# Performance work log

Hardware: AMD Instinct MI355X
Metric: run time of the kernel (lower is better)

Reference implementation:

```python
import jax, jax.numpy as jnp
import numpy as np

MODEL_SIZE = 1024
N_HEAD = 16
D_K = MODEL_SIZE // N_HEAD
B, S = 2, 2048


def setup_inputs() -> dict:
    key = jax.random.key(0)
    ks = jax.random.split(key, 10)
    scale = 1.0 / np.sqrt(MODEL_SIZE)
    q = jax.random.normal(ks[0], (B, S, MODEL_SIZE), dtype=jnp.float32)
    k = jax.random.normal(ks[1], (B, S, MODEL_SIZE), dtype=jnp.float32)
    v = jax.random.normal(ks[2], (B, S, MODEL_SIZE), dtype=jnp.float32)
    mask = jax.random.bernoulli(ks[3], 0.1, (B, S, S))
    Wq = jax.random.normal(ks[4], (MODEL_SIZE, MODEL_SIZE), dtype=jnp.float32) * scale
    bq = jnp.zeros((MODEL_SIZE,), dtype=jnp.float32)
    Wout = jax.random.normal(ks[5], (MODEL_SIZE, MODEL_SIZE), dtype=jnp.float32) * scale
    bout = jnp.zeros((MODEL_SIZE,), dtype=jnp.float32)
    gamma = jnp.ones((MODEL_SIZE,), dtype=jnp.float32)
    beta = jnp.zeros((MODEL_SIZE,), dtype=jnp.float32)
    return {"q": q, "k": k, "v": v, "mask": mask, "Wq": Wq, "bq": bq,
            "Wout": Wout, "bout": bout, "gamma": gamma, "beta": beta}


def _split_heads(x, seq_len):
    # [B, S, D] -> [B, S, h, d_k] -> [B, h, S, d_k] -> [B*h, S, d_k]
    b = x.shape[0]
    return x.reshape(b, seq_len, N_HEAD, D_K).transpose(0, 2, 1, 3).reshape(b * N_HEAD, seq_len, D_K)


def reference(q, k, v, mask, Wq, bq, Wout, bout, gamma, beta):
    residual = q
    len_q, len_k = q.shape[1], k.shape[1]
    # NOTE: faithful to source — linear_q projects q, k AND v.
    qp = _split_heads(q @ Wq.T + bq, len_q)
    kp = _split_heads(k @ Wq.T + bq, len_k)
    vp = _split_heads(v @ Wq.T + bq, len_k)
    # scores: [B*h, len_q, len_k], scale = sqrt(model_size) per source quirk
    attn = jnp.einsum('bqd,bkd->bqk', qp, kp) / jnp.sqrt(jnp.float32(MODEL_SIZE))
    # mask.repeat(h,1,1): tiles head-major -> [h*B, len_q, len_k]
    mask_t = jnp.tile(mask, (N_HEAD, 1, 1))
    attn = jnp.where(mask_t, jnp.float32(-1e18), attn)
    w = jax.nn.softmax(attn, axis=-1)
    out = jnp.einsum('bqk,bkd->bqd', w, vp)  # [B*h, len_q, d_k]
    b = residual.shape[0]
    out = out.reshape(b, N_HEAD, len_q, D_K).transpose(0, 2, 1, 3).reshape(b, len_q, MODEL_SIZE)
    out = out @ Wout.T + bout
    x = residual + out
    mu = jnp.mean(x, axis=-1, keepdims=True)
    var = jnp.var(x, axis=-1, keepdims=True)
    out = (x - mu) / jnp.sqrt(var + 1e-6) * gamma + beta
    return (out, w)
```

## Files before the change

### kernel.cpp

```cpp
#include <hip/hip_runtime.h>
#include <hip/hip_bf16.h>

#define SEQ 2048
#define DIM 1024
#define NH 16
#define DK 64
#define NBH 32
#define MROWS 4096
#define BM 128
#define BN 128
#define BK 32

typedef __attribute__((ext_vector_type(8))) short bf16x8_t;
typedef __attribute__((ext_vector_type(4))) float f32x4_t;

__device__ __forceinline__ unsigned short f2bf(float f) {
  union { float f; unsigned u; } v; v.f = f;
  unsigned r = v.u + 0x7FFFu + ((v.u >> 16) & 1u);
  return (unsigned short)(r >> 16);
}

__device__ __forceinline__ void gload16(const unsigned short* g, unsigned short* l) {
  __builtin_amdgcn_global_load_lds((const __attribute__((address_space(1))) void*)g,
                                   (__attribute__((address_space(3))) void*)l, 16, 0, 0);
}

struct Cvt5 {
  const float* src[5];
  unsigned short* dst[5];
  int n4[5];
};

__global__ __launch_bounds__(256) void cvt5_kernel(Cvt5 P) {
  int i = blockIdx.x * 256 + threadIdx.x;
  int off = 0;
#pragma unroll
  for (int s = 0; s < 5; ++s) {
    int n4 = P.n4[s];
    int j = i - off;
    if (j >= 0 && j < n4) {
      float4 v = reinterpret_cast<const float4*>(P.src[s])[j];
      ushort4 o = make_ushort4(f2bf(v.x), f2bf(v.y), f2bf(v.z), f2bf(v.w));
      reinterpret_cast<ushort4*>(P.dst[s])[j] = o;
    }
    off += n4;
  }
}

__global__ void detect_mask_kernel(const unsigned int* m, int* flag) {
  unsigned acc = 0;
  for (int i = threadIdx.x; i < 2048; i += 64)
    acc |= (m[i] & 0xFFFFFF00u);
  unsigned long long b = __ballot(acc != 0);
  if (threadIdx.x == 0) *flag = (b != 0ull) ? 1 : 0;
}

__global__ __launch_bounds__(256) void cvt_mask_kernel(const void* msrc, unsigned char* mdst, const int* flag) {
  int i = blockIdx.x * 256 + threadIdx.x;
  if (*flag) {
    reinterpret_cast<uchar4*>(mdst)[i] = reinterpret_cast<const uchar4*>(msrc)[i];
  } else {
    int4 v = reinterpret_cast<const int4*>(msrc)[i];
    reinterpret_cast<uchar4*>(mdst)[i] =
        make_uchar4((unsigned char)(v.x != 0), (unsigned char)(v.y != 0),
                    (unsigned char)(v.z != 0), (unsigned char)(v.w != 0));
  }
}

__device__ __forceinline__ void gemm_core_128(const unsigned short* A, const unsigned short* Wb,
                                              unsigned short* AL, unsigned short* BL,
                                              f32x4_t acc[4][4], int wv, int lane,
                                              int wr, int wc, int lr, int lg) {
  for (int k0 = 0; k0 < DIM; k0 += BK) {
    if (k0) __syncthreads();
#pragma unroll
    for (int j = 0; j < 2; ++j) {
      const int e = wv * 1024 + j * 512 + lane * 8;
      const int row = e >> 5, kk = e & 31;
      gload16(A + (size_t)row * DIM + k0 + kk, AL + wv * 1024 + j * 512);
      gload16(Wb + (size_t)row * DIM + k0 + kk, BL + wv * 1024 + j * 512);
    }
    __syncthreads();
    bf16x8_t a[4], b[4];
#pragma unroll
    for (int m = 0; m < 4; ++m)
      a[m] = *reinterpret_cast<const bf16x8_t*>(AL + (wr * 64 + m * 16 + lr) * BK + lg * 8);
#pragma unroll
    for (int n = 0; n < 4; ++n)
      b[n] = *reinterpret_cast<const bf16x8_t*>(BL + (wc * 64 + n * 16 + lr) * BK + lg * 8);
#pragma unroll
    for (int m = 0; m < 4; ++m)
#pragma unroll
      for (int n = 0; n < 4; ++n)
        acc[m][n] = __builtin_amdgcn_mfma_f32_16x16x32_bf16(a[m], b[n], acc[m][n], 0, 0, 0);
  }
}

struct Proj3 {
  const unsigned short* A[3];
  unsigned short* dst[3];
};

__global__ __launch_bounds__(256) void proj_gemm_kernel(Proj3 P, const unsigned short* W, const float* bias) {
  const int mtile = blockIdx.x, ntile = blockIdx.y, which = blockIdx.z;
  const unsigned short* A = P.A[which] + (size_t)(mtile * BM) * DIM;
  const unsigned short* Wb = W + (size_t)(ntile * BN) * DIM;
  __shared__ __align__(16) unsigned short AL[BM * BK];
  __shared__ __align__(16) unsigned short BL[BN * BK];
  const int tid = threadIdx.x;
  const int wv = tid >> 6, lane = tid & 63;
  const int lr = lane & 15, lg = lane >> 4;
  const int wr = wv >> 1, wc = wv & 1;
  f32x4_t acc[4][4] = {};
  gemm_core_128(A, Wb, AL, BL, acc, wv, lane, wr, wc, lr, lg);

  unsigned short* dst = P.dst[which];
#pragma unroll
  for (int n = 0; n < 4; ++n) {
    const int dfull = ntile * BN + wc * 64 + n * 16 + lr;
    const int h = dfull >> 6, d = dfull & 63;
    const float bv = bias[dfull];
#pragma unroll
    for (int m = 0; m < 4; ++m) {
#pragma unroll
      for (int r = 0; r < 4; ++r) {
        const int mg = mtile * BM + wr * 64 + m * 16 + lg * 4 + r;
        const int b_ = mg >> 11, s = mg & (SEQ - 1);
        dst[((size_t)(b_ * NH + h) * SEQ + s) * DK + d] = f2bf(acc[m][n][r] + bv);
      }
    }
  }
}

__global__ __launch_bounds__(256) void out_gemm_kernel(const unsigned short* Ain, const unsigned short* W,
                                                       const float* bias, const float* resid, float* X) {
  const int mtile = blockIdx.x, ntile = blockIdx.y;
  const unsigned short* A = Ain + (size_t)(mtile * BM) * DIM;
  const unsigned short* Wb = W + (size_t)(ntile * BN) * DIM;
  __shared__ __align__(16) unsigned short AL[BM * BK];
  __shared__ __align__(16) unsigned short BL[BN * BK];
  const int tid = threadIdx.x;
  const int wv = tid >> 6, lane = tid & 63;
  const int lr = lane & 15, lg = lane >> 4;
  const int wr = wv >> 1, wc = wv & 1;
  f32x4_t acc[4][4] = {};
  gemm_core_128(A, Wb, AL, BL, acc, wv, lane, wr, wc, lr, lg);

#pragma unroll
  for (int n = 0; n < 4; ++n) {
    const int c = ntile * BN + wc * 64 + n * 16 + lr;
    const float bv = bias[c];
#pragma unroll
    for (int m = 0; m < 4; ++m) {
#pragma unroll
      for (int r = 0; r < 4; ++r) {
        const int mg = mtile * BM + wr * 64 + m * 16 + lg * 4 + r;
        X[(size_t)mg * DIM + c] = acc[m][n][r] + bv + resid[(size_t)mg * DIM + c];
      }
    }
  }
}

__global__ __launch_bounds__(256) void transpose_v_kernel(const unsigned short* vp, unsigned short* vpT) {
  const int stile = blockIdx.x, bh = blockIdx.y;
  const int s0 = stile * 64;
  __shared__ unsigned short ld[64][66];
  const int t = threadIdx.x;
  const int r = t >> 2, c0 = (t & 3) * 16;
  const unsigned short* src = vp + ((size_t)bh * SEQ + s0 + r) * DK + c0;
  bf16x8_t v0 = *reinterpret_cast<const bf16x8_t*>(src);
  bf16x8_t v1 = *reinterpret_cast<const bf16x8_t*>(src + 8);
#pragma unroll
  for (int j = 0; j < 8; ++j) {
    ld[r][c0 + j] = (unsigned short)v0[j];
    ld[r][c0 + 8 + j] = (unsigned short)v1[j];
  }
  __syncthreads();
  bf16x8_t w0, w1;
#pragma unroll
  for (int j = 0; j < 8; ++j) {
    w0[j] = (short)ld[c0 + j][r];
    w1[j] = (short)ld[c0 + 8 + j][r];
  }
  unsigned short* dstp = vpT + ((size_t)bh * DK + r) * SEQ + s0 + c0;
  *reinterpret_cast<bf16x8_t*>(dstp) = w0;
  *reinterpret_cast<bf16x8_t*>(dstp + 8) = w1;
}

__global__ __launch_bounds__(256) void attn_kernel(const unsigned short* qp, const unsigned short* kp,
                                                   const unsigned short* vpT, const unsigned char* maskb,
                                                   float* wout, unsigned short* attn_o) {
  const int qtile = blockIdx.x, bh = blockIdx.y;
  const int wv = threadIdx.x >> 6;
  const int l = threadIdx.x & 63;
  const int lr = l & 15, lg = l >> 4;
  const int qrow0 = qtile * 64 + wv * 16;
  const unsigned short* qptr = qp + ((size_t)bh * SEQ + qrow0 + lr) * DK + lg * 8;
  const bf16x8_t aq0 = *reinterpret_cast<const bf16x8_t*>(qptr);
  const bf16x8_t aq1 = *reinterpret_cast<const bf16x8_t*>(qptr + 32);
  const int crow0 = qrow0 + lg * 4;
  const int mb = bh & 1;
  const unsigned char* mr0 = maskb + ((size_t)mb * SEQ + crow0) * SEQ;
  const unsigned char* mr1 = mr0 + SEQ;
  const unsigned char* mr2 = mr0 + 2 * SEQ;
  const unsigned char* mr3 = mr0 + 3 * SEQ;
  const unsigned short* kbase = kp + (size_t)bh * SEQ * DK + lg * 8;
  const float scale = 0.03125f;

  float s0 = 0.f, s1 = 0.f, s2 = 0.f, s3 = 0.f;
  for (int c0 = 0; c0 < SEQ; c0 += 16) {
    const unsigned short* kpp = kbase + (size_t)(c0 + lr) * DK;
    f32x4_t acc = {0.f, 0.f, 0.f, 0.f};
    acc = __builtin_amdgcn_mfma_f32_16x16x32_bf16(aq0, *reinterpret_cast<const bf16x8_t*>(kpp), acc, 0, 0, 0);
    acc = __builtin_amdgcn_mfma_f32_16x16x32_bf16(aq1, *reinterpret_cast<const bf16x8_t*>(kpp + 32), acc, 0, 0, 0);
    const int kc = c0 + lr;
    s0 += mr0[kc] ? 0.f : __expf(acc[0] * scale);
    s1 += mr1[kc] ? 0.f : __expf(acc[1] * scale);
    s2 += mr2[kc] ? 0.f : __expf(acc[2] * scale);
    s3 += mr3[kc] ? 0.f : __expf(acc[3] * scale);
  }
#pragma unroll
  for (int sh = 1; sh < 16; sh <<= 1) {
    s0 += __shfl_xor(s0, sh);
    s1 += __shfl_xor(s1, sh);
    s2 += __shfl_xor(s2, sh);
    s3 += __shfl_xor(s3, sh);
  }
  const float i0 = 1.f / s0, i1 = 1.f / s1, i2 = 1.f / s2, i3 = 1.f / s3;

  float* wr0 = wout + ((size_t)bh * SEQ + crow0) * SEQ;
  float* wr1 = wr0 + SEQ;
  float* wr2 = wr0 + 2 * SEQ;
  float* wr3 = wr0 + 3 * SEQ;
  const unsigned short* vbase = vpT + (size_t)bh * DK * SEQ + lg * 8;
  __shared__ __align__(16) unsigned short Plds[4][16][32];
  f32x4_t o0 = {0.f, 0.f, 0.f, 0.f}, o1 = o0, o2 = o0, o3 = o0;
  for (int k0 = 0; k0 < SEQ; k0 += 32) {
#pragma unroll
    for (int half = 0; half < 2; ++half) {
      const int c0 = k0 + half * 16;
      const unsigned short* kpp = kbase + (size_t)(c0 + lr) * DK;
      f32x4_t acc = {0.f, 0.f, 0.f, 0.f};
      acc = __builtin_amdgcn_mfma_f32_16x16x32_bf16(aq0, *reinterpret_cast<const bf16x8_t*>(kpp), acc, 0, 0, 0);
      acc = __builtin_amdgcn_mfma_f32_16x16x32_bf16(aq1, *reinterpret_cast<const bf16x8_t*>(kpp + 32), acc, 0, 0, 0);
      const int kc = c0 + lr;
      const float p0 = mr0[kc] ? 0.f : __expf(acc[0] * scale) * i0;
      const float p1 = mr1[kc] ? 0.f : __expf(acc[1] * scale) * i1;
      const float p2 = mr2[kc] ? 0.f : __expf(acc[2] * scale) * i2;
      const float p3 = mr3[kc] ? 0.f : __expf(acc[3] * scale) * i3;
      wr0[kc] = p0;
      wr1[kc] = p1;
      wr2[kc] = p2;
      wr3[kc] = p3;
      Plds[wv][lg * 4 + 0][half * 16 + lr] = f2bf(p0);
      Plds[wv][lg * 4 + 1][half * 16 + lr] = f2bf(p1);
      Plds[wv][lg * 4 + 2][half * 16 + lr] = f2bf(p2);
      Plds[wv][lg * 4 + 3][half * 16 + lr] = f2bf(p3);
    }
    const bf16x8_t pa = *reinterpret_cast<const bf16x8_t*>(&Plds[wv][lr][lg * 8]);
    o0 = __builtin_amdgcn_mfma_f32_16x16x32_bf16(pa, *reinterpret_cast<const bf16x8_t*>(vbase + (size_t)( 0 + lr) * SEQ + k0), o0, 0, 0, 0);
    o1 = __builtin_amdgcn_mfma_f32_16x16x32_bf16(pa, *reinterpret_cast<const bf16x8_t*>(vbase + (size_t)(16 + lr) * SEQ + k0), o1, 0, 0, 0);
    o2 = __builtin_amdgcn_mfma_f32_16x16x32_bf16(pa, *reinterpret_cast<const bf16x8_t*>(vbase + (size_t)(32 + lr) * SEQ + k0), o2, 0, 0, 0);
    o3 = __builtin_amdgcn_mfma_f32_16x16x32_bf16(pa, *reinterpret_cast<const bf16x8_t*>(vbase + (size_t)(48 + lr) * SEQ + k0), o3, 0, 0, 0);
  }
  const int b = bh >> 4, h = bh & 15;
  unsigned short* obase = attn_o + ((size_t)b * SEQ + crow0) * DIM + h * DK;
#pragma unroll
  for (int r = 0; r < 4; ++r) {
    unsigned short* orow = obase + (size_t)r * DIM;
    orow[ 0 + lr] = f2bf(o0[r]);
    orow[16 + lr] = f2bf(o1[r]);
    orow[32 + lr] = f2bf(o2[r]);
    orow[48 + lr] = f2bf(o3[r]);
  }
}

__global__ __launch_bounds__(256) void ln_kernel(const float* X, const float* gamma, const float* beta, float* out) {
  const int row = blockIdx.x;
  const int t = threadIdx.x;
  float4 v = reinterpret_cast<const float4*>(X + (size_t)row * DIM)[t];
  float s1 = v.x + v.y + v.z + v.w;
  float s2 = v.x * v.x + v.y * v.y + v.z * v.z + v.w * v.w;
#pragma unroll
  for (int sh = 1; sh < 64; sh <<= 1) {
    s1 += __shfl_xor(s1, sh);
    s2 += __shfl_xor(s2, sh);
  }
  __shared__ float p1[4], p2[4];
  if ((t & 63) == 0) { p1[t >> 6] = s1; p2[t >> 6] = s2; }
  __syncthreads();
  s1 = p1[0] + p1[1] + p1[2] + p1[3];
  s2 = p2[0] + p2[1] + p2[2] + p2[3];
  const float mu = s1 * (1.f / DIM);
  const float var = s2 * (1.f / DIM) - mu * mu;
  const float rstd = rsqrtf(var + 1e-6f);
  float4 g = reinterpret_cast<const float4*>(gamma)[t];
  float4 be = reinterpret_cast<const float4*>(beta)[t];
  float4 o;
  o.x = (v.x - mu) * rstd * g.x + be.x;
  o.y = (v.y - mu) * rstd * g.y + be.y;
  o.z = (v.z - mu) * rstd * g.z + be.z;
  o.w = (v.w - mu) * rstd * g.w + be.w;
  reinterpret_cast<float4*>(out + (size_t)row * DIM)[t] = o;
}

extern "C" void kernel_launch(void* const* d_in, const int* in_sizes, int n_in,
                              void* d_out, int out_size, void* d_ws, size_t ws_size,
                              hipStream_t stream) {
  const float* q     = (const float*)d_in[0];
  const float* k     = (const float*)d_in[1];
  const float* v     = (const float*)d_in[2];
  const void*  mask  = d_in[3];
  const float* Wq    = (const float*)d_in[4];
  const float* bq    = (const float*)d_in[5];
  const float* Wout  = (const float*)d_in[6];
  const float* bout  = (const float*)d_in[7];
  const float* gamma = (const float*)d_in[8];
  const float* beta  = (const float*)d_in[9];

  float* out0 = (float*)d_out;
  float* wout = out0 + (size_t)2 * SEQ * DIM;

  char* ws = (char*)d_ws;
  size_t off = 0;
  auto alloc = [&](size_t bytes) -> char* {
    char* p = ws + off;
    off += (bytes + 255) & ~(size_t)255;
    return p;
  };
  int* flag            = (int*)alloc(256);
  unsigned short* qb   = (unsigned short*)alloc((size_t)MROWS * DIM * 2);
  unsigned short* kb   = (unsigned short*)alloc((size_t)MROWS * DIM * 2);
  unsigned short* vb   = (unsigned short*)alloc((size_t)MROWS * DIM * 2);
  unsigned short* Wqb  = (unsigned short*)alloc((size_t)DIM * DIM * 2);
  unsigned short* Wob  = (unsigned short*)alloc((size_t)DIM * DIM * 2);
  unsigned short* qp   = (unsigned short*)alloc((size_t)NBH * SEQ * DK * 2);
  unsigned short* kp   = (unsigned short*)alloc((size_t)NBH * SEQ * DK * 2);
  unsigned short* vp   = (unsigned short*)alloc((size_t)NBH * SEQ * DK * 2);
  unsigned short* vpT  = (unsigned short*)alloc((size_t)NBH * SEQ * DK * 2);
  unsigned short* ao   = (unsigned short*)alloc((size_t)MROWS * DIM * 2);
  unsigned char* maskb = (unsigned char*)alloc((size_t)2 * SEQ * SEQ);
  float* X             = (float*)alloc((size_t)MROWS * DIM * 4);

  Cvt5 C;
  C.src[0] = q;    C.dst[0] = qb;  C.n4[0] = MROWS * DIM / 4;
  C.src[1] = k;    C.dst[1] = kb;  C.n4[1] = MROWS * DIM / 4;
  C.src[2] = v;    C.dst[2] = vb;  C.n4[2] = MROWS * DIM / 4;
  C.src[3] = Wq;   C.dst[3] = Wqb; C.n4[3] = DIM * DIM / 4;
  C.src[4] = Wout; C.dst[4] = Wob; C.n4[4] = DIM * DIM / 4;
  const int totalN4 = 3 * (MROWS * DIM / 4) + 2 * (DIM * DIM / 4);
  cvt5_kernel<<<(totalN4 + 255) / 256, 256, 0, stream>>>(C);

  detect_mask_kernel<<<1, 64, 0, stream>>>((const unsigned int*)mask, flag);
  cvt_mask_kernel<<<(2 * SEQ * SEQ / 4 + 255) / 256, 256, 0, stream>>>(mask, maskb, flag);

  Proj3 P;
  P.A[0] = qb; P.dst[0] = qp;
  P.A[1] = kb; P.dst[1] = kp;
  P.A[2] = vb; P.dst[2] = vp;
  proj_gemm_kernel<<<dim3(MROWS / BM, DIM / BN, 3), 256, 0, stream>>>(P, Wqb, bq);

  transpose_v_kernel<<<dim3(SEQ / 64, NBH), 256, 0, stream>>>(vp, vpT);

  attn_kernel<<<dim3(SEQ / 64, NBH), 256, 0, stream>>>(qp, kp, vpT, maskb, wout, ao);

  out_gemm_kernel<<<dim3(MROWS / BM, DIM / BN), 256, 0, stream>>>(ao, Wob, bout, q, X);

  ln_kernel<<<MROWS, 256, 0, stream>>>(X, gamma, beta, out0);
}
```

Measured before the change: 1.111 ms.

## Swap MFMA operand order for row-contiguous vectorized stores, prefetch K/V, remap attention blocks to XCDs

Swaps the A/B operands of every MFMA so that each lane holds four consecutive columns of a single row. This lets the projection epilogue, the output-GEMM epilogue, the attention-probability writes and the attention output use 4-wide vector stores in place of scattered scalar stores. In the attention kernel it also software-pipelines the K-fragment loads one step ahead, issues the V loads early, reads the mask as uchar4 and pads the P tile in LDS. It remaps the block index so that heads group onto XCDs for L2 locality. The main target is the heavily strided 128 MB fp32 probability write and the uncoalesced epilogues, at the cost of extra registers for the prefetched fragments.

```diff
diff --git a/kernel.cpp b/kernel.cpp
--- a/kernel.cpp
+++ b/kernel.cpp
@@ -12,6 +12,7 @@
 #define BK 32
 
 typedef __attribute__((ext_vector_type(8))) short bf16x8_t;
+typedef __attribute__((ext_vector_type(4))) short bf16x4_t;
 typedef __attribute__((ext_vector_type(4))) float f32x4_t;
 
 __device__ __forceinline__ unsigned short f2bf(float f) {
@@ -92,7 +93,7 @@
     for (int m = 0; m < 4; ++m)
 #pragma unroll
       for (int n = 0; n < 4; ++n)
-        acc[m][n] = __builtin_amdgcn_mfma_f32_16x16x32_bf16(a[m], b[n], acc[m][n], 0, 0, 0);
+        acc[m][n] = __builtin_amdgcn_mfma_f32_16x16x32_bf16(b[n], a[m], acc[m][n], 0, 0, 0);
   }
 }
 
@@ -115,19 +116,22 @@
   gemm_core_128(A, Wb, AL, BL, acc, wv, lane, wr, wc, lr, lg);
 
   unsigned short* dst = P.dst[which];
-#pragma unroll
-  for (int n = 0; n < 4; ++n) {
-    const int dfull = ntile * BN + wc * 64 + n * 16 + lr;
-    const int h = dfull >> 6, d = dfull & 63;
-    const float bv = bias[dfull];
-#pragma unroll
-    for (int m = 0; m < 4; ++m) {
-#pragma unroll
-      for (int r = 0; r < 4; ++r) {
-        const int mg = mtile * BM + wr * 64 + m * 16 + lg * 4 + r;
-        const int b_ = mg >> 11, s = mg & (SEQ - 1);
-        dst[((size_t)(b_ * NH + h) * SEQ + s) * DK + d] = f2bf(acc[m][n][r] + bv);
-      }
+  const int h = ntile * 2 + wc;
+#pragma unroll
+  for (int m = 0; m < 4; ++m) {
+    const int mg = mtile * BM + wr * 64 + m * 16 + lr;
+    const int b_ = mg >> 11, s = mg & (SEQ - 1);
+    unsigned short* drow = dst + ((size_t)(b_ * NH + h) * SEQ + s) * DK;
+#pragma unroll
+    for (int n = 0; n < 4; ++n) {
+      const int d0 = n * 16 + lg * 4;
+      const float4 bv = *reinterpret_cast<const float4*>(&bias[ntile * BN + wc * 64 + d0]);
+      bf16x4_t o;
+      o[0] = (short)f2bf(acc[m][n][0] + bv.x);
+      o[1] = (short)f2bf(acc[m][n][1] + bv.y);
+      o[2] = (short)f2bf(acc[m][n][2] + bv.z);
+      o[3] = (short)f2bf(acc[m][n][3] + bv.w);
+      *reinterpret_cast<bf16x4_t*>(drow + d0) = o;
     }
   }
 }
@@ -147,16 +151,21 @@
   gemm_core_128(A, Wb, AL, BL, acc, wv, lane, wr, wc, lr, lg);
 
 #pragma unroll
-  for (int n = 0; n < 4; ++n) {
-    const int c = ntile * BN + wc * 64 + n * 16 + lr;
-    const float bv = bias[c];
-#pragma unroll
-    for (int m = 0; m < 4; ++m) {
-#pragma unroll
-      for (int r = 0; r < 4; ++r) {
-        const int mg = mtile * BM + wr * 64 + m * 16 + lg * 4 + r;
-        X[(size_t)mg * DIM + c] = acc[m][n][r] + bv + resid[(size_t)mg * DIM + c];
-      }
+  for (int m = 0; m < 4; ++m) {
+    const int mg = mtile * BM + wr * 64 + m * 16 + lr;
+    float* xrow = X + (size_t)mg * DIM;
+    const float* rrow = resid + (size_t)mg * DIM;
+#pragma unroll
+    for (int n = 0; n < 4; ++n) {
+      const int c0 = ntile * BN + wc * 64 + n * 16 + lg * 4;
+      const float4 bv = *reinterpret_cast<const float4*>(&bias[c0]);
+      const float4 rv = *reinterpret_cast<const float4*>(&rrow[c0]);
+      float4 o;
+      o.x = acc[m][n][0] + bv.x + rv.x;
+      o.y = acc[m][n][1] + bv.y + rv.y;
+      o.z = acc[m][n][2] + bv.z + rv.z;
+      o.w = acc[m][n][3] + bv.w + rv.w;
+      *reinterpret_cast<float4*>(&xrow[c0]) = o;
     }
   }
 }
@@ -190,88 +199,111 @@
 __global__ __launch_bounds__(256) void attn_kernel(const unsigned short* qp, const unsigned short* kp,
                                                    const unsigned short* vpT, const unsigned char* maskb,
                                                    float* wout, unsigned short* attn_o) {
-  const int qtile = blockIdx.x, bh = blockIdx.y;
+  const int lin = blockIdx.y * gridDim.x + blockIdx.x;
+  const int xcd = lin & 7, chunk = lin >> 3;
+  const int bh = xcd * 4 + (chunk & 3);
+  const int qtile = chunk >> 2;
   const int wv = threadIdx.x >> 6;
   const int l = threadIdx.x & 63;
   const int lr = l & 15, lg = l >> 4;
   const int qrow0 = qtile * 64 + wv * 16;
   const unsigned short* qptr = qp + ((size_t)bh * SEQ + qrow0 + lr) * DK + lg * 8;
-  const bf16x8_t aq0 = *reinterpret_cast<const bf16x8_t*>(qptr);
-  const bf16x8_t aq1 = *reinterpret_cast<const bf16x8_t*>(qptr + 32);
-  const int crow0 = qrow0 + lg * 4;
+  const bf16x8_t bq0 = *reinterpret_cast<const bf16x8_t*>(qptr);
+  const bf16x8_t bq1 = *reinterpret_cast<const bf16x8_t*>(qptr + 32);
   const int mb = bh & 1;
-  const unsigned char* mr0 = maskb + ((size_t)mb * SEQ + crow0) * SEQ;
-  const unsigned char* mr1 = mr0 + SEQ;
-  const unsigned char* mr2 = mr0 + 2 * SEQ;
-  const unsigned char* mr3 = mr0 + 3 * SEQ;
+  const unsigned char* mrow = maskb + ((size_t)mb * SEQ + qrow0 + lr) * SEQ;
   const unsigned short* kbase = kp + (size_t)bh * SEQ * DK + lg * 8;
   const float scale = 0.03125f;
 
-  float s0 = 0.f, s1 = 0.f, s2 = 0.f, s3 = 0.f;
-  for (int c0 = 0; c0 < SEQ; c0 += 16) {
-    const unsigned short* kpp = kbase + (size_t)(c0 + lr) * DK;
-    f32x4_t acc = {0.f, 0.f, 0.f, 0.f};
-    acc = __builtin_amdgcn_mfma_f32_16x16x32_bf16(aq0, *reinterpret_cast<const bf16x8_t*>(kpp), acc, 0, 0, 0);
-    acc = __builtin_amdgcn_mfma_f32_16x16x32_bf16(aq1, *reinterpret_cast<const bf16x8_t*>(kpp + 32), acc, 0, 0, 0);
-    const int kc = c0 + lr;
-    s0 += mr0[kc] ? 0.f : __expf(acc[0] * scale);
-    s1 += mr1[kc] ? 0.f : __expf(acc[1] * scale);
-    s2 += mr2[kc] ? 0.f : __expf(acc[2] * scale);
-    s3 += mr3[kc] ? 0.f : __expf(acc[3] * scale);
-  }
-#pragma unroll
-  for (int sh = 1; sh < 16; sh <<= 1) {
-    s0 += __shfl_xor(s0, sh);
-    s1 += __shfl_xor(s1, sh);
-    s2 += __shfl_xor(s2, sh);
-    s3 += __shfl_xor(s3, sh);
-  }
-  const float i0 = 1.f / s0, i1 = 1.f / s1, i2 = 1.f / s2, i3 = 1.f / s3;
-
-  float* wr0 = wout + ((size_t)bh * SEQ + crow0) * SEQ;
-  float* wr1 = wr0 + SEQ;
-  float* wr2 = wr0 + 2 * SEQ;
-  float* wr3 = wr0 + 3 * SEQ;
+#define LDK(c) *reinterpret_cast<const bf16x8_t*>(kbase + (size_t)((c) + lr) * DK)
+#define LDK2(c) *reinterpret_cast<const bf16x8_t*>(kbase + (size_t)((c) + lr) * DK + 32)
+
+  float sum = 0.f;
+  {
+    bf16x8_t kA0 = LDK(0), kA1 = LDK2(0);
+    for (int c0 = 0; c0 < SEQ; c0 += 32) {
+      bf16x8_t kB0 = LDK(c0 + 16), kB1 = LDK2(c0 + 16);
+      {
+        f32x4_t s4 = {0.f, 0.f, 0.f, 0.f};
+        s4 = __builtin_amdgcn_mfma_f32_16x16x32_bf16(kA0, bq0, s4, 0, 0, 0);
+        s4 = __builtin_amdgcn_mfma_f32_16x16x32_bf16(kA1, bq1, s4, 0, 0, 0);
+        uchar4 mv = *reinterpret_cast<const uchar4*>(mrow + c0 + lg * 4);
+        sum += (mv.x ? 0.f : __expf(s4[0] * scale)) + (mv.y ? 0.f : __expf(s4[1] * scale))
+             + (mv.z ? 0.f : __expf(s4[2] * scale)) + (mv.w ? 0.f : __expf(s4[3] * scale));
+      }
+      const int nc = (c0 + 32) & (SEQ - 1);
+      kA0 = LDK(nc); kA1 = LDK2(nc);
+      {
+        f32x4_t s4 = {0.f, 0.f, 0.f, 0.f};
+        s4 = __builtin_amdgcn_mfma_f32_16x16x32_bf16(kB0, bq0, s4, 0, 0, 0);
+        s4 = __builtin_amdgcn_mfma_f32_16x16x32_bf16(kB1, bq1, s4, 0, 0, 0);
+        uchar4 mv = *reinterpret_cast<const uchar4*>(mrow + c0 + 16 + lg * 4);
+        sum += (mv.x ? 0.f : __expf(s4[0] * scale)) + (mv.y ? 0.f : __expf(s4[1] * scale))
+             + (mv.z ? 0.f : __expf(s4[2] * scale)) + (mv.w ? 0.f : __expf(s4[3] * scale));
+      }
+    }
+  }
+  sum += __shfl_xor(sum, 16);
+  sum += __shfl_xor(sum, 32);
+  const float inv = 1.f / sum;
+
+  float* wrow = wout + ((size_t)bh * SEQ + qrow0 + lr) * SEQ;
   const unsigned short* vbase = vpT + (size_t)bh * DK * SEQ + lg * 8;
-  __shared__ __align__(16) unsigned short Plds[4][16][32];
+  __shared__ __align__(16) unsigned short Plds[4][16][40];
   f32x4_t o0 = {0.f, 0.f, 0.f, 0.f}, o1 = o0, o2 = o0, o3 = o0;
-  for (int k0 = 0; k0 < SEQ; k0 += 32) {
-#pragma unroll
-    for (int half = 0; half < 2; ++half) {
-      const int c0 = k0 + half * 16;
-      const unsigned short* kpp = kbase + (size_t)(c0 + lr) * DK;
-      f32x4_t acc = {0.f, 0.f, 0.f, 0.f};
-      acc = __builtin_amdgcn_mfma_f32_16x16x32_bf16(aq0, *reinterpret_cast<const bf16x8_t*>(kpp), acc, 0, 0, 0);
-      acc = __builtin_amdgcn_mfma_f32_16x16x32_bf16(aq1, *reinterpret_cast<const bf16x8_t*>(kpp + 32), acc, 0, 0, 0);
-      const int kc = c0 + lr;
-      const float p0 = mr0[kc] ? 0.f : __expf(acc[0] * scale) * i0;
-      const float p1 = mr1[kc] ? 0.f : __expf(acc[1] * scale) * i1;
-      const float p2 = mr2[kc] ? 0.f : __expf(acc[2] * scale) * i2;
-      const float p3 = mr3[kc] ? 0.f : __expf(acc[3] * scale) * i3;
-      wr0[kc] = p0;
-      wr1[kc] = p1;
-      wr2[kc] = p2;
-      wr3[kc] = p3;
-      Plds[wv][lg * 4 + 0][half * 16 + lr] = f2bf(p0);
-      Plds[wv][lg * 4 + 1][half * 16 + lr] = f2bf(p1);
-      Plds[wv][lg * 4 + 2][half * 16 + lr] = f2bf(p2);
-      Plds[wv][lg * 4 + 3][half * 16 + lr] = f2bf(p3);
-    }
-    const bf16x8_t pa = *reinterpret_cast<const bf16x8_t*>(&Plds[wv][lr][lg * 8]);
-    o0 = __builtin_amdgcn_mfma_f32_16x16x32_bf16(pa, *reinterpret_cast<const bf16x8_t*>(vbase + (size_t)( 0 + lr) * SEQ + k0), o0, 0, 0, 0);
-    o1 = __builtin_amdgcn_mfma_f32_16x16x32_bf16(pa, *reinterpret_cast<const bf16x8_t*>(vbase + (size_t)(16 + lr) * SEQ + k0), o1, 0, 0, 0);
-    o2 = __builtin_amdgcn_mfma_f32_16x16x32_bf16(pa, *reinterpret_cast<const bf16x8_t*>(vbase + (size_t)(32 + lr) * SEQ + k0), o2, 0, 0, 0);
-    o3 = __builtin_amdgcn_mfma_f32_16x16x32_bf16(pa, *reinterpret_cast<const bf16x8_t*>(vbase + (size_t)(48 + lr) * SEQ + k0), o3, 0, 0, 0);
-  }
-  const int b = bh >> 4, h = bh & 15;
-  unsigned short* obase = attn_o + ((size_t)b * SEQ + crow0) * DIM + h * DK;
-#pragma unroll
-  for (int r = 0; r < 4; ++r) {
-    unsigned short* orow = obase + (size_t)r * DIM;
-    orow[ 0 + lr] = f2bf(o0[r]);
-    orow[16 + lr] = f2bf(o1[r]);
-    orow[32 + lr] = f2bf(o2[r]);
-    orow[48 + lr] = f2bf(o3[r]);
+
+#define COMP(c0base, kk0, kk1, w16)                                                     \
+  {                                                                                     \
+    f32x4_t s4 = {0.f, 0.f, 0.f, 0.f};                                                  \
+    s4 = __builtin_amdgcn_mfma_f32_16x16x32_bf16(kk0, bq0, s4, 0, 0, 0);                \
+    s4 = __builtin_amdgcn_mfma_f32_16x16x32_bf16(kk1, bq1, s4, 0, 0, 0);                \
+    uchar4 mv = *reinterpret_cast<const uchar4*>(mrow + (c0base) + lg * 4);             \
+    float4 pv;                                                                          \
+    pv.x = mv.x ? 0.f : __expf(s4[0] * scale) * inv;                                    \
+    pv.y = mv.y ? 0.f : __expf(s4[1] * scale) * inv;                                    \
+    pv.z = mv.z ? 0.f : __expf(s4[2] * scale) * inv;                                    \
+    pv.w = mv.w ? 0.f : __expf(s4[3] * scale) * inv;                                    \
+    *reinterpret_cast<float4*>(wrow + (c0base) + lg * 4) = pv;                          \
+    bf16x4_t pb;                                                                        \
+    pb[0] = (short)f2bf(pv.x); pb[1] = (short)f2bf(pv.y);                               \
+    pb[2] = (short)f2bf(pv.z); pb[3] = (short)f2bf(pv.w);                               \
+    *reinterpret_cast<bf16x4_t*>(&Plds[wv][lr][(w16) * 16 + lg * 4]) = pb;              \
+  }
+
+  {
+    bf16x8_t kA0 = LDK(0), kA1 = LDK2(0);
+    for (int k0 = 0; k0 < SEQ; k0 += 32) {
+      const bf16x8_t va0 = *reinterpret_cast<const bf16x8_t*>(vbase + (size_t)( 0 + lr) * SEQ + k0);
+      const bf16x8_t va1 = *reinterpret_cast<const bf16x8_t*>(vbase + (size_t)(16 + lr) * SEQ + k0);
+      const bf16x8_t va2 = *reinterpret_cast<const bf16x8_t*>(vbase + (size_t)(32 + lr) * SEQ + k0);
+      const bf16x8_t va3 = *reinterpret_cast<const bf16x8_t*>(vbase + (size_t)(48 + lr) * SEQ + k0);
+      bf16x8_t kB0 = LDK(k0 + 16), kB1 = LDK2(k0 + 16);
+      COMP(k0, kA0, kA1, 0);
+      const int nc = (k0 + 32) & (SEQ - 1);
+      kA0 = LDK(nc); kA1 = LDK2(nc);
+      COMP(k0 + 16, kB0, kB1, 1);
+      const bf16x8_t pfrag = *reinterpret_cast<const bf16x8_t*>(&Plds[wv][lr][lg * 8]);
+      o0 = __builtin_amdgcn_mfma_f32_16x16x32_bf16(va0, pfrag, o0, 0, 0, 0);
+      o1 = __builtin_amdgcn_mfma_f32_16x16x32_bf16(va1, pfrag, o1, 0, 0, 0);
+      o2 = __builtin_amdgcn_mfma_f32_16x16x32_bf16(va2, pfrag, o2, 0, 0, 0);
+      o3 = __builtin_amdgcn_mfma_f32_16x16x32_bf16(va3, pfrag, o3, 0, 0, 0);
+    }
+  }
+#undef COMP
+#undef LDK
+#undef LDK2
+
+  const int b_ = bh >> 4, h = bh & 15;
+  unsigned short* obase = attn_o + ((size_t)b_ * SEQ + qrow0 + lr) * DIM + h * DK + lg * 4;
+  f32x4_t oacc[4] = {o0, o1, o2, o3};
+#pragma unroll
+  for (int t = 0; t < 4; ++t) {
+    bf16x4_t ov;
+    ov[0] = (short)f2bf(oacc[t][0]);
+    ov[1] = (short)f2bf(oacc[t][1]);
+    ov[2] = (short)f2bf(oacc[t][2]);
+    ov[3] = (short)f2bf(oacc[t][3]);
+    *reinterpret_cast<bf16x4_t*>(obase + t * 16) = ov;
   }
 }
 
```

Result: no change. 1.119 ms (+0.8%).
